# Optimization experiments

Measured on AMD Instinct MI355X. Metric: run time of the kernel, lower is better.

## Reference

```python
import jax, jax.numpy as jnp
import numpy as np

N_HEAD = 16
N_KV = 4
HEAD_DIM = 128
WINDOW = 1024
SINK = 4
THETA = 10000.0


def _rope_cos_sin(T, dim, theta, dtype):
    inv_freq = 1.0 / (theta ** (jnp.arange(0, dim, 2, dtype=jnp.float32) / dim))
    t = jnp.arange(T, dtype=jnp.float32)
    ang = jnp.outer(t, inv_freq)  # [T, dim/2]
    return jnp.cos(ang).astype(dtype), jnp.sin(ang).astype(dtype)


def _apply_rope(x, cos, sin):
    # x: [B, H, T, D]; cos/sin: [T, D/2]
    d2 = x.shape[-1] // 2
    x1, x2 = x[..., :d2], x[..., d2:]
    return jnp.concatenate([x1 * cos - x2 * sin, x2 * cos + x1 * sin], axis=-1)


def setup_inputs() -> dict:
    key = jax.random.key(0)
    ks = jax.random.split(key, 5)
    B, T, C = 2, 2048, 2048
    x = jax.random.normal(ks[0], (B, T, C), dtype=jnp.float32)
    s = 0.02
    wq = jax.random.normal(ks[1], (C, C), dtype=jnp.float32) * s
    wk = jax.random.normal(ks[2], (N_KV * HEAD_DIM, C), dtype=jnp.float32) * s
    wv = jax.random.normal(ks[3], (N_KV * HEAD_DIM, C), dtype=jnp.float32) * s
    wo = jax.random.normal(ks[4], (C, C), dtype=jnp.float32) * s
    return {"x": x, "wq": wq, "wk": wk, "wv": wv, "wo": wo}


def reference(x, wq, wk, wv, wo):
    B, T, C = x.shape
    # QKV projections (Linear with weight [out, in], no bias)
    q = (x @ wq.T).reshape(B, T, N_HEAD, HEAD_DIM).transpose(0, 2, 1, 3)  # [B,H,T,D]
    k = (x @ wk.T).reshape(B, T, N_KV, HEAD_DIM).transpose(0, 2, 1, 3)    # [B,Hkv,T,D]
    v = (x @ wv.T).reshape(B, T, N_KV, HEAD_DIM).transpose(0, 2, 1, 3)

    cos, sin = _rope_cos_sin(T, HEAD_DIM, THETA, x.dtype)
    q = _apply_rope(q, cos, sin)
    k = _apply_rope(k, cos, sin)

    # GQA: repeat kv heads to match query heads (repeat_interleave on head dim)
    rep = N_HEAD // N_KV
    k = jnp.repeat(k, rep, axis=1)
    v = jnp.repeat(v, rep, axis=1)

    # causal + sliding window + attention sink mask
    i = jnp.arange(T)[:, None]
    j = jnp.arange(T)[None, :]
    allowed = (j <= i) & (((i - j) <= WINDOW) | (j < SINK))
    bias = jnp.where(allowed, 0.0, -jnp.inf).astype(x.dtype)  # [T,T]

    scale = 1.0 / np.sqrt(HEAD_DIM)
    att = jnp.einsum("bhqd,bhkd->bhqk", q, k) * scale + bias
    att = jax.nn.softmax(att, axis=-1)
    y = jnp.einsum("bhqk,bhkd->bhqd", att, v)  # [B,H,T,D]
    y = y.transpose(0, 2, 1, 3).reshape(B, T, C)
    return y @ wo.T
```

## Files before the change

kernel.cpp:

```cpp
#include <hip/hip_runtime.h>
#include <hip/hip_bf16.h>

typedef __bf16 bf16x8 __attribute__((ext_vector_type(8)));
typedef __bf16 bf16x4 __attribute__((ext_vector_type(4)));
typedef float  f32x4  __attribute__((ext_vector_type(4)));
typedef unsigned int uint4v __attribute__((ext_vector_type(4)));

#define NB     2
#define TT     2048
#define CC     2048
#define NH     16
#define NKV    4
#define HD     128
#define WIN    1024
#define SINKN  4
#define QSCALE2 (0.08838834764831845f * 1.44269504088896340f)

__device__ __forceinline__ void lds_load16(const void* g, void* l) {
    __builtin_amdgcn_global_load_lds(
        (__attribute__((address_space(1))) void*)const_cast<void*>(g),
        (__attribute__((address_space(3))) void*)l, 16, 0, 0);
}

__device__ __forceinline__ unsigned pack2bf(float a, float b) {
    __bf16 x = (__bf16)a, y = (__bf16)b;
    unsigned short ux = __builtin_bit_cast(unsigned short, x);
    unsigned short uy = __builtin_bit_cast(unsigned short, y);
    return (unsigned)ux | ((unsigned)uy << 16);
}

__device__ __forceinline__ float fast_exp2(float x) {
    float r;
    asm("v_exp_f32 %0, %1" : "=v"(r) : "v"(x));
    return r;
}

__global__ void prolog_kernel(const float* __restrict__ x,
                              const float* __restrict__ wq, const float* __restrict__ wk,
                              const float* __restrict__ wv, const float* __restrict__ wo,
                              __bf16* __restrict__ xb, __bf16* __restrict__ Wall,
                              float* __restrict__ cosT, float* __restrict__ sinT) {
    const int g = blockIdx.x * 256 + threadIdx.x;
    if (g < 2097152) {
        const int idx = g * 4;
        const float4 v = *(const float4*)(x + idx);
        bf16x4 o;
        o[0] = (__bf16)v.x; o[1] = (__bf16)v.y; o[2] = (__bf16)v.z; o[3] = (__bf16)v.w;
        *(bf16x4*)(xb + idx) = o;
    } else if (g < 4718592) {
        const int idx = (g - 2097152) * 4;
        const float* src; int off;
        if (idx < 4194304)      { src = wq; off = idx; }
        else if (idx < 5242880) { src = wk; off = idx - 4194304; }
        else if (idx < 6291456) { src = wv; off = idx - 5242880; }
        else                    { src = wo; off = idx - 6291456; }
        const float4 v = *(const float4*)(src + off);
        bf16x4 o;
        o[0] = (__bf16)v.x; o[1] = (__bf16)v.y; o[2] = (__bf16)v.z; o[3] = (__bf16)v.w;
        *(bf16x4*)(Wall + idx) = o;
    } else {
        const int i = g - 4718592;
        const int t = i >> 6, d = i & 63;
        const float inv_freq = 1.0f / powf(10000.0f, (float)d * (1.0f / 64.0f));
        const float ang = (float)t * inv_freq;
        cosT[i] = cosf(ang);
        sinT[i] = sinf(ang);
    }
}

__global__ void scatter_vt_kernel(const __bf16* __restrict__ qkv,
                                  const float* __restrict__ cosT,
                                  const float* __restrict__ sinT,
                                  __bf16* __restrict__ Qo,
                                  __bf16* __restrict__ Ko,
                                  __bf16* __restrict__ Vt) {
    __shared__ __bf16 tile[64][72];
    if (blockIdx.x < 2560) {
        const int job = blockIdx.x * 256 + threadIdx.x;
        int m, d8, base_off; __bf16* outp; float scale;
        if (job < 524288) {
            m = job >> 7;
            const int pj = job & 127;
            const int hh = pj >> 3; d8 = pj & 7;
            base_off = hh * 128;
            const int b = m >> 11, t = m & 2047;
            outp = Qo + ((size_t)(b * NH + hh) * TT + t) * HD + d8 * 8;
            scale = QSCALE2;
        } else {
            const int j2 = job - 524288;
            m = j2 >> 5;
            const int pj = j2 & 31;
            const int g = pj >> 3; d8 = pj & 7;
            base_off = 2048 + g * 128;
            const int b = m >> 11, t = m & 2047;
            outp = Ko + ((size_t)(b * NKV + g) * TT + t) * HD + d8 * 8;
            scale = 1.0f;
        }
        const int t = m & 2047;
        const __bf16* row = qkv + (size_t)m * 3072 + base_off + d8 * 8;
        const bf16x8 x1 = *(const bf16x8*)row;
        const bf16x8 x2 = *(const bf16x8*)(row + 64);
        const float4 c0 = *(const float4*)(cosT + t * 64 + d8 * 8);
        const float4 c1 = *(const float4*)(cosT + t * 64 + d8 * 8 + 4);
        const float4 s0 = *(const float4*)(sinT + t * 64 + d8 * 8);
        const float4 s1 = *(const float4*)(sinT + t * 64 + d8 * 8 + 4);
        const float cs[8] = {c0.x, c0.y, c0.z, c0.w, c1.x, c1.y, c1.z, c1.w};
        const float sn[8] = {s0.x, s0.y, s0.z, s0.w, s1.x, s1.y, s1.z, s1.w};
        bf16x8 o1, o2;
#pragma unroll
        for (int e = 0; e < 8; ++e) {
            const float a = (float)x1[e], bb = (float)x2[e];
            o1[e] = (__bf16)((a * cs[e] - bb * sn[e]) * scale);
            o2[e] = (__bf16)((bb * cs[e] + a * sn[e]) * scale);
        }
        *(bf16x8*)outp = o1;
        *(bf16x8*)(outp + 64) = o2;
    } else {
        const int idx2 = blockIdx.x - 2560;
        const int t0 = (idx2 & 31) << 6, d0 = ((idx2 >> 5) & 1) << 6, bkv = idx2 >> 6;
        const int b = bkv >> 2, g = bkv & 3;
        const int r = threadIdx.x >> 2, cg = threadIdx.x & 3;
        const __bf16* src = qkv + (size_t)(b * TT + t0 + r) * 3072 + 2560 + g * 128 + d0 + cg * 16;
        *(bf16x8*)&tile[r][cg * 16]     = *(const bf16x8*)src;
        *(bf16x8*)&tile[r][cg * 16 + 8] = *(const bf16x8*)(src + 8);
        __syncthreads();
        __bf16* dst = Vt + ((size_t)bkv * HD + d0 + r) * TT + t0 + cg * 16;
        bf16x8 o0, o1;
#pragma unroll
        for (int c2 = 0; c2 < 8; ++c2) {
            o0[c2] = tile[cg * 16 + c2][r];
            o1[c2] = tile[cg * 16 + 8 + c2][r];
        }
        *(bf16x8*)dst = o0;
        *(bf16x8*)(dst + 8) = o1;
    }
}

template <int OUT_BF16>
__global__ __launch_bounds__(512, 2) void gemm_bt8(const __bf16* __restrict__ A,
                                                   const __bf16* __restrict__ Bm,
                                                   void* __restrict__ C,
                                                   int M, int N, int K) {
    __shared__ __align__(16) __bf16 lA[2][256 * 64];
    __shared__ __align__(16) __bf16 lB[2][256 * 64];
    const int tid = threadIdx.x;
    const int lane = tid & 63;
    const int w = tid >> 6;
    const int wm = w >> 2, wn = w & 3;
    const int nbn = N >> 8;
    const int nwg = (M >> 8) * nbn;
    const int chunk = nwg >> 3;
    const int swz = (blockIdx.x & 7) * chunk + (blockIdx.x >> 3);
    const int bm = swz / nbn, bn = swz % nbn;
    const int m0 = bm << 8, n0 = bn << 8;
    const int lr = lane & 15, lh = lane >> 4;
    const int NT = K >> 6;

    auto stageA = [&](int kt, int buf, int i) {
        const int d = i * 8192 + tid * 16;
        const int row = d >> 7;
        const int colb = (d & 127) ^ ((row & 7) << 4);
        lds_load16(A + (size_t)(m0 + row) * K + kt * 64 + (colb >> 1),
                   (char*)lA[buf] + i * 8192 + w * 1024);
    };
    auto stageB = [&](int kt, int buf, int i) {
        const int d = i * 8192 + tid * 16;
        const int row = d >> 7;
        const int colb = (d & 127) ^ ((row & 7) << 4);
        lds_load16(Bm + (size_t)(n0 + row) * K + kt * 64 + (colb >> 1),
                   (char*)lB[buf] + i * 8192 + w * 1024);
    };

    f32x4 acc[8][4] = {};

#pragma unroll
    for (int i = 0; i < 4; ++i) stageA(0, 0, i);
#pragma unroll
    for (int i = 0; i < 4; ++i) stageB(0, 0, i);
    asm volatile("s_waitcnt vmcnt(0)" ::: "memory");
    __syncthreads();

    for (int kt = 0; kt < NT; ++kt) {
        const int cur = kt & 1, nxt = cur ^ 1;
        const bool pf = (kt + 1 < NT);
        const char* bA = (const char*)lA[cur];
        const char* bB = (const char*)lB[cur];

        bf16x8 aF[4][2], b0[2][2], b1[2][2];
#pragma unroll
        for (int mf = 0; mf < 4; ++mf)
#pragma unroll
            for (int ks = 0; ks < 2; ++ks) {
                const int row = wm * 128 + mf * 16 + lr;
                const int cb = (ks * 64 + lh * 16) ^ ((row & 7) << 4);
                aF[mf][ks] = *(const bf16x8*)(bA + row * 128 + cb);
            }
#pragma unroll
        for (int nf = 0; nf < 2; ++nf)
#pragma unroll
            for (int ks = 0; ks < 2; ++ks) {
                const int row = wn * 64 + nf * 16 + lr;
                const int cb = (ks * 64 + lh * 16) ^ ((row & 7) << 4);
                b0[nf][ks] = *(const bf16x8*)(bB + row * 128 + cb);
            }
        if (pf) { stageA(kt + 1, nxt, 0); stageA(kt + 1, nxt, 1); stageA(kt + 1, nxt, 2); stageA(kt + 1, nxt, 3); }
        __builtin_amdgcn_s_setprio(1);
#pragma unroll
        for (int mf = 0; mf < 4; ++mf)
#pragma unroll
            for (int nf = 0; nf < 2; ++nf)
#pragma unroll
                for (int ks = 0; ks < 2; ++ks)
                    acc[mf][nf] = __builtin_amdgcn_mfma_f32_16x16x32_bf16(aF[mf][ks], b0[nf][ks], acc[mf][nf], 0, 0, 0);
        __builtin_amdgcn_s_setprio(0);

#pragma unroll
        for (int nf = 0; nf < 2; ++nf)
#pragma unroll
            for (int ks = 0; ks < 2; ++ks) {
                const int row = wn * 64 + 32 + nf * 16 + lr;
                const int cb = (ks * 64 + lh * 16) ^ ((row & 7) << 4);
                b1[nf][ks] = *(const bf16x8*)(bB + row * 128 + cb);
            }
        if (pf) { stageB(kt + 1, nxt, 0); stageB(kt + 1, nxt, 1); stageB(kt + 1, nxt, 2); stageB(kt + 1, nxt, 3); }
        __builtin_amdgcn_s_setprio(1);
#pragma unroll
        for (int mf = 0; mf < 4; ++mf)
#pragma unroll
            for (int nf = 0; nf < 2; ++nf)
#pragma unroll
                for (int ks = 0; ks < 2; ++ks)
                    acc[mf][nf + 2] = __builtin_amdgcn_mfma_f32_16x16x32_bf16(aF[mf][ks], b1[nf][ks], acc[mf][nf + 2], 0, 0, 0);
        __builtin_amdgcn_s_setprio(0);

#pragma unroll
        for (int mf = 0; mf < 4; ++mf)
#pragma unroll
            for (int ks = 0; ks < 2; ++ks) {
                const int row = wm * 128 + 64 + mf * 16 + lr;
                const int cb = (ks * 64 + lh * 16) ^ ((row & 7) << 4);
                aF[mf][ks] = *(const bf16x8*)(bA + row * 128 + cb);
            }
        __builtin_amdgcn_s_setprio(1);
#pragma unroll
        for (int mf = 0; mf < 4; ++mf)
#pragma unroll
            for (int nf = 0; nf < 2; ++nf)
#pragma unroll
                for (int ks = 0; ks < 2; ++ks)
                    acc[mf + 4][nf] = __builtin_amdgcn_mfma_f32_16x16x32_bf16(aF[mf][ks], b0[nf][ks], acc[mf + 4][nf], 0, 0, 0);
        __builtin_amdgcn_s_setprio(0);

        __builtin_amdgcn_s_setprio(1);
#pragma unroll
        for (int mf = 0; mf < 4; ++mf)
#pragma unroll
            for (int nf = 0; nf < 2; ++nf)
#pragma unroll
                for (int ks = 0; ks < 2; ++ks)
                    acc[mf + 4][nf + 2] = __builtin_amdgcn_mfma_f32_16x16x32_bf16(aF[mf][ks], b1[nf][ks], acc[mf + 4][nf + 2], 0, 0, 0);
        __builtin_amdgcn_s_setprio(0);

        asm volatile("s_waitcnt vmcnt(0)" ::: "memory");
        __syncthreads();
    }

#pragma unroll
    for (int mf = 0; mf < 8; ++mf)
#pragma unroll
        for (int nf = 0; nf < 4; ++nf)
#pragma unroll
            for (int r = 0; r < 4; ++r) {
                const size_t row = m0 + wm * 128 + mf * 16 + lh * 4 + r;
                const size_t col = n0 + wn * 64 + nf * 16 + lr;
                if (OUT_BF16) ((__bf16*)C)[row * N + col] = (__bf16)acc[mf][nf][r];
                else          ((float*)C)[row * N + col]  = acc[mf][nf][r];
            }
}

template <int OUT_BF16>
__global__ __launch_bounds__(256, 2) void gemm_bt(const __bf16* __restrict__ A,
                                                  const __bf16* __restrict__ Bm,
                                                  void* __restrict__ C,
                                                  int M, int N, int K) {
    __shared__ __align__(16) __bf16 lA[2][128 * 64];
    __shared__ __align__(16) __bf16 lB[2][128 * 64];
    const int tid = threadIdx.x;
    const int lane = tid & 63;
    const int w = tid >> 6;
    const int wr = w >> 1, wc = w & 1;
    const int nbn = N >> 7;
    const int nwg = (M >> 7) * nbn;
    const int chunk = nwg >> 3;
    const int swz = (blockIdx.x & 7) * chunk + (blockIdx.x >> 3);
    const int bm = swz / nbn, bn = swz % nbn;
    const int m0 = bm << 7, n0 = bn << 7;
    const int lr = lane & 15, lh = lane >> 4;
    f32x4 acc[4][4] = {};

    auto stage = [&](int k0, int buf) {
#pragma unroll
        for (int i = 0; i < 4; ++i) {
            const int d = i * 4096 + tid * 16;
            const int row = d >> 7;
            const int colb = (d & 127) ^ ((row & 7) << 4);
            lds_load16(A + (size_t)(m0 + row) * K + k0 + (colb >> 1),
                       (char*)lA[buf] + i * 4096 + w * 1024);
            lds_load16(Bm + (size_t)(n0 + row) * K + k0 + (colb >> 1),
                       (char*)lB[buf] + i * 4096 + w * 1024);
        }
    };

    stage(0, 0);
    asm volatile("s_waitcnt vmcnt(0)" ::: "memory");
    __syncthreads();

    const int NT = K >> 6;
    for (int kt = 0; kt < NT; ++kt) {
        const int buf = kt & 1;
        if (kt + 1 < NT) stage((kt + 1) << 6, buf ^ 1);

        const char* bA = (const char*)lA[buf];
        const char* bB = (const char*)lB[buf];
        bf16x8 af[4][2], bfr[4][2];
#pragma unroll
        for (int t = 0; t < 4; ++t)
#pragma unroll
            for (int ks = 0; ks < 2; ++ks) {
                const int rowa = wr * 64 + t * 16 + lr;
                const int cba = (ks * 64 + lh * 16) ^ ((rowa & 7) << 4);
                af[t][ks] = *(const bf16x8*)(bA + rowa * 128 + cba);
                const int rowb = wc * 64 + t * 16 + lr;
                const int cbb = (ks * 64 + lh * 16) ^ ((rowb & 7) << 4);
                bfr[t][ks] = *(const bf16x8*)(bB + rowb * 128 + cbb);
            }
#pragma unroll
        for (int mt = 0; mt < 4; ++mt)
#pragma unroll
            for (int nt = 0; nt < 4; ++nt)
#pragma unroll
                for (int ks = 0; ks < 2; ++ks)
                    acc[mt][nt] = __builtin_amdgcn_mfma_f32_16x16x32_bf16(af[mt][ks], bfr[nt][ks], acc[mt][nt], 0, 0, 0);

        asm volatile("s_waitcnt vmcnt(0)" ::: "memory");
        __syncthreads();
    }

    const int r0 = (lane >> 4) * 4;
#pragma unroll
    for (int mt = 0; mt < 4; ++mt)
#pragma unroll
        for (int nt = 0; nt < 4; ++nt)
#pragma unroll
            for (int r = 0; r < 4; ++r) {
                const size_t row = m0 + wr * 64 + mt * 16 + r0 + r;
                const size_t col = n0 + wc * 64 + nt * 16 + lr;
                if (OUT_BF16) ((__bf16*)C)[row * N + col] = (__bf16)acc[mt][nt][r];
                else          ((float*)C)[row * N + col]  = acc[mt][nt][r];
            }
}

__global__ __launch_bounds__(512, 4) void attn_kernel(const __bf16* __restrict__ Q,
                                                      const __bf16* __restrict__ Kg,
                                                      const __bf16* __restrict__ Vt,
                                                      __bf16* __restrict__ Y) {
    const int id = blockIdx.x;
    const int grp = id & 7;
    const int pos = id >> 3;
    const int kv = grp & 3, b = grp >> 2;
    const int qt2 = 63 - pos;
    const int q0 = qt2 << 5;
    const int tid = threadIdx.x, lane = tid & 63, w = tid >> 6;
    const int lr = lane & 15, lh = lane >> 4;
    const int hh = w >> 1;
    const int h  = kv * 4 + hh;
    const int wh = w & 1;

    __shared__ __align__(16) __bf16 lK[64 * 128];
    __shared__ __align__(16) __bf16 lV[128 * 64];

    bf16x8 qf[4];
    {
        const __bf16* Qb = Q + ((size_t)(b * NH + h) * TT + q0 + wh * 16) * HD;
#pragma unroll
        for (int kc = 0; kc < 4; ++kc)
            qf[kc] = *(const bf16x8*)(Qb + lr * HD + kc * 32 + lh * 8);
    }

    f32x4 acc[8] = {};
    float mrun = -1e30f, lrun = 0.f;
    const int iq = q0 + wh * 16 + lr;

    const __bf16* Kb = Kg + (size_t)(b * NKV + kv) * TT * HD;
    const __bf16* Vb = Vt + (size_t)(b * NKV + kv) * HD * TT;
    const int jend = qt2 >> 1;
    const int jsw  = (q0 > WIN) ? ((q0 - WIN) >> 6) : 0;

    for (int jb = 0; jb <= jend; ++jb) {
        if (jb > 0 && jb < jsw) continue;
        const int j0 = jb << 6;
        __syncthreads();
#pragma unroll
        for (int L = 0; L < 2; ++L) {
            const int o = L * 8192 + w * 1024 + lane * 16;
            {
                const int row = o >> 8;
                const int colb = (o & 255) ^ ((row & 7) << 4);
                lds_load16(Kb + (size_t)(j0 + row) * HD + (colb >> 1), (char*)lK + L * 8192 + w * 1024);
            }
            {
                const int row = o >> 7;
                const int colb = (o & 127) ^ ((row & 7) << 4);
                lds_load16(Vb + (size_t)row * TT + j0 + (colb >> 1), (char*)lV + L * 8192 + w * 1024);
            }
        }
        asm volatile("s_waitcnt vmcnt(0)" ::: "memory");
        __syncthreads();

        f32x4 s4[4];
#pragma unroll
        for (int nt = 0; nt < 4; ++nt) {
            f32x4 s = {0.f, 0.f, 0.f, 0.f};
#pragma unroll
            for (int kc = 0; kc < 4; ++kc) {
                const int row = nt * 16 + lr;
                const int colb = ((kc * 32 + lh * 8) << 1) ^ ((row & 7) << 4);
                const bf16x8 kf = *(const bf16x8*)((const char*)lK + row * 256 + colb);
                s = __builtin_amdgcn_mfma_f32_16x16x32_bf16(kf, qf[kc], s, 0, 0, 0);
            }
            s4[nt] = s;
        }

        const bool fullTile = (j0 + 63 <= q0) && (q0 + 31 - j0 <= WIN);
        if (!fullTile) {
#pragma unroll
            for (int nt = 0; nt < 4; ++nt)
#pragma unroll
                for (int r = 0; r < 4; ++r) {
                    const int j = j0 + nt * 16 + lh * 4 + r;
                    const bool ok = (j <= iq) && ((iq - j <= WIN) || (j < SINKN));
                    if (!ok) s4[nt][r] = -1e30f;
                }
        }

        float mx = s4[0][0];
#pragma unroll
        for (int nt = 0; nt < 4; ++nt)
#pragma unroll
            for (int r = 0; r < 4; ++r) mx = fmaxf(mx, s4[nt][r]);
        mx = fmaxf(mx, __shfl_xor(mx, 16, 64));
        mx = fmaxf(mx, __shfl_xor(mx, 32, 64));

        if (!__all(mx - mrun <= 11.53f)) {
            const float mnew = fmaxf(mrun, mx);
            const float corr = fast_exp2(mrun - mnew);
            mrun = mnew;
            lrun *= corr;
#pragma unroll
            for (int r = 0; r < 4; ++r) {
                const float c = __shfl(corr, lh * 4 + r, 64);
#pragma unroll
                for (int dt = 0; dt < 8; ++dt) acc[dt][r] *= c;
            }
        }

        float rsum = 0.f;
#pragma unroll
        for (int nt = 0; nt < 4; ++nt)
#pragma unroll
            for (int r = 0; r < 4; ++r) {
                const float p = fast_exp2(s4[nt][r] - mrun);
                s4[nt][r] = p;
                rsum += p;
            }
        rsum += __shfl_xor(rsum, 16, 64);
        rsum += __shfl_xor(rsum, 32, 64);
        lrun += rsum;

        unsigned pw[4][2];
#pragma unroll
        for (int nt = 0; nt < 4; ++nt) {
            pw[nt][0] = pack2bf(s4[nt][0], s4[nt][1]);
            pw[nt][1] = pack2bf(s4[nt][2], s4[nt][3]);
        }
        bf16x8 pa[2];
#pragma unroll
        for (int kc = 0; kc < 2; ++kc) {
            uint4v wv;
#pragma unroll
            for (int widx = 0; widx < 4; ++widx) {
                const int m = widx & 1;
                const int srcl = lr + 16 * ((2 * lh + (widx >> 1)) & 3);
                const int wA = __shfl((int)pw[2 * kc][m], srcl, 64);
                const int wB = __shfl((int)pw[2 * kc + 1][m], srcl, 64);
                wv[widx] = (unsigned)((lh & 2) ? wB : wA);
            }
            pa[kc] = __builtin_bit_cast(bf16x8, wv);
        }

#pragma unroll
        for (int dt = 0; dt < 8; ++dt) {
#pragma unroll
            for (int kc = 0; kc < 2; ++kc) {
                const int row = dt * 16 + lr;
                const int colb = ((kc * 32 + lh * 8) << 1) ^ ((row & 7) << 4);
                const bf16x8 vf = *(const bf16x8*)((const char*)lV + row * 128 + colb);
                acc[dt] = __builtin_amdgcn_mfma_f32_16x16x32_bf16(pa[kc], vf, acc[dt], 0, 0, 0);
            }
        }
    }

    const float inv = 1.f / lrun;
#pragma unroll
    for (int r = 0; r < 4; ++r) {
        const float invr = __shfl(inv, lh * 4 + r, 64);
        const int trow = q0 + wh * 16 + lh * 4 + r;
        __bf16* Yp = Y + ((size_t)b * TT + trow) * CC + h * HD;
#pragma unroll
        for (int dt = 0; dt < 8; ++dt)
            Yp[dt * 16 + lr] = (__bf16)(acc[dt][r] * invr);
    }
}

extern "C" void kernel_launch(void* const* d_in, const int* in_sizes, int n_in,
                              void* d_out, int out_size, void* d_ws, size_t ws_size,
                              hipStream_t stream) {
    const float* x  = (const float*)d_in[0];
    const float* wq = (const float*)d_in[1];
    const float* wk = (const float*)d_in[2];
    const float* wv = (const float*)d_in[3];
    const float* wo = (const float*)d_in[4];
    float* out = (float*)d_out;

    char* ws = (char*)d_ws;
    size_t off = 0;
    auto alloc = [&](size_t bytes) { char* p = ws + off; off += bytes; return p; };
    __bf16* xb   = (__bf16*)alloc(16777216);
    __bf16* Wall = (__bf16*)alloc(12582912);
    __bf16* wob  = (__bf16*)alloc(8388608);
    __bf16* qkv  = (__bf16*)alloc(25165824);
    __bf16* Qs   = (__bf16*)alloc(16777216);
    __bf16* Ks   = (__bf16*)alloc(4194304);
    __bf16* Vts  = (__bf16*)alloc(4194304);
    float*  cosT = (float*)alloc(524288);
    float*  sinT = (float*)alloc(524288);
    __bf16* Yb = xb;

    prolog_kernel<<<18944, 256, 0, stream>>>(x, wq, wk, wv, wo, xb, Wall, cosT, sinT);
    gemm_bt8<1><<<dim3(16 * 12), 512, 0, stream>>>(xb, Wall, qkv, 4096, 3072, 2048);
    scatter_vt_kernel<<<3072, 256, 0, stream>>>(qkv, cosT, sinT, Qs, Ks, Vts);
    attn_kernel<<<dim3(512), 512, 0, stream>>>(Qs, Ks, Vts, Yb);
    gemm_bt<0><<<dim3(32 * 16), 256, 0, stream>>>(Yb, wob, out, 4096, 2048, 2048);
}
```

Before: 168.0 us.

## Switch attention kernel to 32x32x16 MFMA with one wave per head

```diff
diff --git a/kernel.cpp b/kernel.cpp
--- a/kernel.cpp
+++ b/kernel.cpp
@@ -4,6 +4,7 @@
 typedef __bf16 bf16x8 __attribute__((ext_vector_type(8)));
 typedef __bf16 bf16x4 __attribute__((ext_vector_type(4)));
 typedef float  f32x4  __attribute__((ext_vector_type(4)));
+typedef float  f32x16 __attribute__((ext_vector_type(16)));
 typedef unsigned int uint4v __attribute__((ext_vector_type(4)));
 
 #define NB     2
@@ -360,7 +361,7 @@
             }
 }
 
-__global__ __launch_bounds__(512, 4) void attn_kernel(const __bf16* __restrict__ Q,
+__global__ __launch_bounds__(256, 2) void attn_kernel(const __bf16* __restrict__ Q,
                                                       const __bf16* __restrict__ Kg,
                                                       const __bf16* __restrict__ Vt,
                                                       __bf16* __restrict__ Y) {
@@ -371,25 +372,23 @@
     const int qt2 = 63 - pos;
     const int q0 = qt2 << 5;
     const int tid = threadIdx.x, lane = tid & 63, w = tid >> 6;
-    const int lr = lane & 15, lh = lane >> 4;
-    const int hh = w >> 1;
-    const int h  = kv * 4 + hh;
-    const int wh = w & 1;
+    const int l31 = lane & 31, hi = lane >> 5;
+    const int h  = kv * 4 + w;
 
     __shared__ __align__(16) __bf16 lK[64 * 128];
     __shared__ __align__(16) __bf16 lV[128 * 64];
 
-    bf16x8 qf[4];
+    bf16x8 qf[8];
     {
-        const __bf16* Qb = Q + ((size_t)(b * NH + h) * TT + q0 + wh * 16) * HD;
-#pragma unroll
-        for (int kc = 0; kc < 4; ++kc)
-            qf[kc] = *(const bf16x8*)(Qb + lr * HD + kc * 32 + lh * 8);
+        const __bf16* Qb = Q + ((size_t)(b * NH + h) * TT + q0) * HD;
+#pragma unroll
+        for (int c = 0; c < 8; ++c)
+            qf[c] = *(const bf16x8*)(Qb + l31 * HD + c * 16 + hi * 8);
     }
 
-    f32x4 acc[8] = {};
+    f32x16 acc[4] = {};
     float mrun = -1e30f, lrun = 0.f;
-    const int iq = q0 + wh * 16 + lr;
+    const int iq = q0 + l31;
 
     const __bf16* Kb = Kg + (size_t)(b * NKV + kv) * TT * HD;
     const __bf16* Vb = Vt + (size_t)(b * NKV + kv) * HD * TT;
@@ -401,54 +400,55 @@
         const int j0 = jb << 6;
         __syncthreads();
 #pragma unroll
-        for (int L = 0; L < 2; ++L) {
-            const int o = L * 8192 + w * 1024 + lane * 16;
+        for (int i = 0; i < 4; ++i) {
+            const int o = i * 4096 + tid * 16;
             {
                 const int row = o >> 8;
                 const int colb = (o & 255) ^ ((row & 7) << 4);
-                lds_load16(Kb + (size_t)(j0 + row) * HD + (colb >> 1), (char*)lK + L * 8192 + w * 1024);
+                lds_load16(Kb + (size_t)(j0 + row) * HD + (colb >> 1),
+                           (char*)lK + i * 4096 + w * 1024);
             }
             {
                 const int row = o >> 7;
                 const int colb = (o & 127) ^ ((row & 7) << 4);
-                lds_load16(Vb + (size_t)row * TT + j0 + (colb >> 1), (char*)lV + L * 8192 + w * 1024);
+                lds_load16(Vb + (size_t)row * TT + j0 + (colb >> 1),
+                           (char*)lV + i * 4096 + w * 1024);
             }
         }
         asm volatile("s_waitcnt vmcnt(0)" ::: "memory");
         __syncthreads();
 
-        f32x4 s4[4];
-#pragma unroll
-        for (int nt = 0; nt < 4; ++nt) {
-            f32x4 s = {0.f, 0.f, 0.f, 0.f};
-#pragma unroll
-            for (int kc = 0; kc < 4; ++kc) {
-                const int row = nt * 16 + lr;
-                const int colb = ((kc * 32 + lh * 8) << 1) ^ ((row & 7) << 4);
-                const bf16x8 kf = *(const bf16x8*)((const char*)lK + row * 256 + colb);
-                s = __builtin_amdgcn_mfma_f32_16x16x32_bf16(kf, qf[kc], s, 0, 0, 0);
-            }
-            s4[nt] = s;
+        f32x16 st[2];
+#pragma unroll
+        for (int kt2 = 0; kt2 < 2; ++kt2) {
+            f32x16 s = {};
+#pragma unroll
+            for (int c = 0; c < 8; ++c) {
+                const int row = kt2 * 32 + l31;
+                const int cb = (c * 32 + hi * 16) ^ ((row & 7) << 4);
+                const bf16x8 kf = *(const bf16x8*)((const char*)lK + row * 256 + cb);
+                s = __builtin_amdgcn_mfma_f32_32x32x16_bf16(kf, qf[c], s, 0, 0, 0);
+            }
+            st[kt2] = s;
         }
 
         const bool fullTile = (j0 + 63 <= q0) && (q0 + 31 - j0 <= WIN);
         if (!fullTile) {
 #pragma unroll
-            for (int nt = 0; nt < 4; ++nt)
-#pragma unroll
-                for (int r = 0; r < 4; ++r) {
-                    const int j = j0 + nt * 16 + lh * 4 + r;
+            for (int kt2 = 0; kt2 < 2; ++kt2)
+#pragma unroll
+                for (int rr = 0; rr < 16; ++rr) {
+                    const int j = j0 + kt2 * 32 + (rr & 3) + 8 * (rr >> 2) + 4 * hi;
                     const bool ok = (j <= iq) && ((iq - j <= WIN) || (j < SINKN));
-                    if (!ok) s4[nt][r] = -1e30f;
+                    if (!ok) st[kt2][rr] = -1e30f;
                 }
         }
 
-        float mx = s4[0][0];
-#pragma unroll
-        for (int nt = 0; nt < 4; ++nt)
-#pragma unroll
-            for (int r = 0; r < 4; ++r) mx = fmaxf(mx, s4[nt][r]);
-        mx = fmaxf(mx, __shfl_xor(mx, 16, 64));
+        float mx = st[0][0];
+#pragma unroll
+        for (int kt2 = 0; kt2 < 2; ++kt2)
+#pragma unroll
+            for (int rr = 0; rr < 16; ++rr) mx = fmaxf(mx, st[kt2][rr]);
         mx = fmaxf(mx, __shfl_xor(mx, 32, 64));
 
         if (!__all(mx - mrun <= 11.53f)) {
@@ -457,69 +457,71 @@
             mrun = mnew;
             lrun *= corr;
 #pragma unroll
-            for (int r = 0; r < 4; ++r) {
-                const float c = __shfl(corr, lh * 4 + r, 64);
-#pragma unroll
-                for (int dt = 0; dt < 8; ++dt) acc[dt][r] *= c;
+            for (int rr = 0; rr < 16; ++rr) {
+                const float cq = __shfl(corr, (rr & 3) + 8 * (rr >> 2) + 4 * hi, 64);
+#pragma unroll
+                for (int dt = 0; dt < 4; ++dt) acc[dt][rr] *= cq;
             }
         }
 
         float rsum = 0.f;
 #pragma unroll
-        for (int nt = 0; nt < 4; ++nt)
-#pragma unroll
-            for (int r = 0; r < 4; ++r) {
-                const float p = fast_exp2(s4[nt][r] - mrun);
-                s4[nt][r] = p;
+        for (int kt2 = 0; kt2 < 2; ++kt2)
+#pragma unroll
+            for (int rr = 0; rr < 16; ++rr) {
+                const float p = fast_exp2(st[kt2][rr] - mrun);
+                st[kt2][rr] = p;
                 rsum += p;
             }
-        rsum += __shfl_xor(rsum, 16, 64);
         rsum += __shfl_xor(rsum, 32, 64);
         lrun += rsum;
 
-        unsigned pw[4][2];
-#pragma unroll
-        for (int nt = 0; nt < 4; ++nt) {
-            pw[nt][0] = pack2bf(s4[nt][0], s4[nt][1]);
-            pw[nt][1] = pack2bf(s4[nt][2], s4[nt][3]);
-        }
-        bf16x8 pa[2];
-#pragma unroll
-        for (int kc = 0; kc < 2; ++kc) {
-            uint4v wv;
-#pragma unroll
-            for (int widx = 0; widx < 4; ++widx) {
-                const int m = widx & 1;
-                const int srcl = lr + 16 * ((2 * lh + (widx >> 1)) & 3);
-                const int wA = __shfl((int)pw[2 * kc][m], srcl, 64);
-                const int wB = __shfl((int)pw[2 * kc + 1][m], srcl, 64);
-                wv[widx] = (unsigned)((lh & 2) ? wB : wA);
-            }
-            pa[kc] = __builtin_bit_cast(bf16x8, wv);
-        }
-
-#pragma unroll
-        for (int dt = 0; dt < 8; ++dt) {
-#pragma unroll
-            for (int kc = 0; kc < 2; ++kc) {
-                const int row = dt * 16 + lr;
-                const int colb = ((kc * 32 + lh * 8) << 1) ^ ((row & 7) << 4);
-                const bf16x8 vf = *(const bf16x8*)((const char*)lV + row * 128 + colb);
-                acc[dt] = __builtin_amdgcn_mfma_f32_16x16x32_bf16(pa[kc], vf, acc[dt], 0, 0, 0);
+        bf16x8 pa[4];
+#pragma unroll
+        for (int c = 0; c < 4; ++c) {
+            const int kt2 = c >> 1, g = c & 1, base = 8 * g;
+            const unsigned u1a = pack2bf(st[kt2][base + 0], st[kt2][base + 1]);
+            const unsigned u1b = pack2bf(st[kt2][base + 2], st[kt2][base + 3]);
+            const unsigned u2a = pack2bf(st[kt2][base + 4], st[kt2][base + 5]);
+            const unsigned u2b = pack2bf(st[kt2][base + 6], st[kt2][base + 7]);
+            const unsigned p1a = (unsigned)__shfl_xor((int)u1a, 32, 64);
+            const unsigned p1b = (unsigned)__shfl_xor((int)u1b, 32, 64);
+            const unsigned p2a = (unsigned)__shfl_xor((int)u2a, 32, 64);
+            const unsigned p2b = (unsigned)__shfl_xor((int)u2b, 32, 64);
+            uint4v uv;
+            uv[0] = hi ? p2a : u1a;
+            uv[1] = hi ? p2b : u1b;
+            uv[2] = hi ? u2a : p1a;
+            uv[3] = hi ? u2b : p1b;
+            pa[c] = __builtin_bit_cast(bf16x8, uv);
+        }
+
+#pragma unroll
+        for (int dt = 0; dt < 4; ++dt) {
+            const int row = dt * 32 + l31;
+            const int swzr = (row & 7) << 4;
+#pragma unroll
+            for (int c = 0; c < 4; ++c) {
+                const int cb = (c * 32 + hi * 16) ^ swzr;
+                const bf16x8 vf = *(const bf16x8*)((const char*)lV + row * 128 + cb);
+                acc[dt] = __builtin_amdgcn_mfma_f32_32x32x16_bf16(pa[c], vf, acc[dt], 0, 0, 0);
             }
         }
     }
 
     const float inv = 1.f / lrun;
-#pragma unroll
-    for (int r = 0; r < 4; ++r) {
-        const float invr = __shfl(inv, lh * 4 + r, 64);
-        const int trow = q0 + wh * 16 + lh * 4 + r;
-        __bf16* Yp = Y + ((size_t)b * TT + trow) * CC + h * HD;
-#pragma unroll
-        for (int dt = 0; dt < 8; ++dt)
-            Yp[dt * 16 + lr] = (__bf16)(acc[dt][r] * invr);
-    }
+    float invq[16];
+#pragma unroll
+    for (int rr = 0; rr < 16; ++rr)
+        invq[rr] = __shfl(inv, (rr & 3) + 8 * (rr >> 2) + 4 * hi, 64);
+#pragma unroll
+    for (int dt = 0; dt < 4; ++dt)
+#pragma unroll
+        for (int rr = 0; rr < 16; ++rr) {
+            const int qrow = (rr & 3) + 8 * (rr >> 2) + 4 * hi;
+            Y[((size_t)b * TT + q0 + qrow) * CC + h * HD + dt * 32 + l31] =
+                (__bf16)(acc[dt][rr] * invq[rr]);
+        }
 }
 
 extern "C" void kernel_launch(void* const* d_in, const int* in_sizes, int n_in,
@@ -549,6 +551,6 @@
     prolog_kernel<<<18944, 256, 0, stream>>>(x, wq, wk, wv, wo, xb, Wall, cosT, sinT);
     gemm_bt8<1><<<dim3(16 * 12), 512, 0, stream>>>(xb, Wall, qkv, 4096, 3072, 2048);
     scatter_vt_kernel<<<3072, 256, 0, stream>>>(qkv, cosT, sinT, Qs, Ks, Vts);
-    attn_kernel<<<dim3(512), 512, 0, stream>>>(Qs, Ks, Vts, Yb);
+    attn_kernel<<<dim3(512), 256, 0, stream>>>(Qs, Ks, Vts, Yb);
     gemm_bt<0><<<dim3(32 * 16), 256, 0, stream>>>(Yb, wob, out, 4096, 2048, 2048);
 }
```

Result: faster. 160.5 us (median of 3 runs) (-4.5%).
